# Performance work log

Hardware: AMD Instinct MI355X
Metric: run time of the kernel (lower is better)

The kernel has to match this reference:

```python
import jax, jax.numpy as jnp
import numpy as np

N_NODES = 50000
N_EDGES = 1600000
N_FEAT = 4
N_GRAPHS = 128
K = 5


def setup_inputs() -> dict:
    key = jax.random.key(0)
    ks = jax.random.split(key, 16)
    x = jax.random.normal(ks[0], (N_NODES, N_FEAT), dtype=jnp.float32)
    edge_index = jax.random.randint(ks[1], (2, N_EDGES), 0, N_NODES, dtype=jnp.int64)
    batch = jnp.sort(jax.random.randint(ks[2], (N_NODES,), 0, N_GRAPHS, dtype=jnp.int64))
    def lin(k, shape):
        fan_in = shape[-2]
        return jax.random.normal(k, shape, dtype=jnp.float32) / np.sqrt(fan_in)
    return {
        "x": x,
        "edge_index": edge_index,
        "batch": batch,
        "num_graphs": N_GRAPHS,
        "W1": lin(ks[3], (K, N_FEAT, 32)), "b1": jnp.zeros((32,), jnp.float32),
        "W2": lin(ks[4], (K, 32, 64)),     "b2": jnp.zeros((64,), jnp.float32),
        "W3": lin(ks[5], (K, 64, 64)),     "b3": jnp.zeros((64,), jnp.float32),
        "fcw1": lin(ks[6], (64, 32)), "fcb1": jnp.zeros((32,), jnp.float32),
        "fcw2": lin(ks[7], (32, 1)),  "fcb2": jnp.zeros((1,), jnp.float32),
    }


def _cheb_conv(h, src, dst, w, Wk, b, n_nodes):
    # PyG ChebConv with sym norm, lambda_max=2:
    #   L_hat h = scatter_add(w_e * h[src_e] -> dst_e), w_e = -dinv[src]*dinv[dst]
    def L(z):
        return jax.ops.segment_sum(w[:, None] * z[src], dst, num_segments=n_nodes)
    Tx0 = h
    Tx1 = L(h)
    out = jnp.einsum('nf,fo->no', Tx0, Wk[0]) + jnp.einsum('nf,fo->no', Tx1, Wk[1])
    for k in range(2, Wk.shape[0]):
        Tx2 = 2.0 * L(Tx1) - Tx0
        out = out + jnp.einsum('nf,fo->no', Tx2, Wk[k])
        Tx0, Tx1 = Tx1, Tx2
    return out + b


def reference(x, edge_index, batch, num_graphs, W1, b1, W2, b2, W3, b3,
              fcw1, fcb1, fcw2, fcb2):
    n = x.shape[0]
    src, dst = edge_index[0], edge_index[1]
    # remove self loops (PyG ChebConv does remove_self_loops first)
    ew = (src != dst).astype(x.dtype)
    deg = jax.ops.segment_sum(ew, src, num_segments=n)
    dinv = jnp.where(deg > 0, jax.lax.rsqrt(jnp.where(deg > 0, deg, 1.0)), 0.0)
    w = -ew * dinv[src] * dinv[dst]  # scaled Laplacian off-diagonal; diagonal is 0

    h = jax.nn.relu(_cheb_conv(x, src, dst, w, W1, b1, n))
    h = jax.nn.relu(_cheb_conv(h, src, dst, w, W2, b2, n))
    h = jax.nn.relu(_cheb_conv(h, src, dst, w, W3, b3, n))

    # global_mean_pool over graph segments
    sums = jax.ops.segment_sum(h, batch, num_segments=num_graphs)
    cnts = jax.ops.segment_sum(jnp.ones((n,), h.dtype), batch, num_segments=num_graphs)
    pooled = sums / jnp.maximum(cnts, 1.0)[:, None]

    h = jax.nn.relu(pooled @ fcw1 + fcb1)
    return h @ fcw2 + fcb2
```

## Files before the change

### kernel.cpp

```cpp
#include <hip/hip_runtime.h>


constexpr int N_NODES  = 50000;
constexpr int N_EDGES  = 1600000;
constexpr int N_GRAPHS = 128;

constexpr int N16  = N_NODES * 16;
constexpr int SB32 = (N_NODES + 31) / 32;

constexpr int NB_H = 256;
constexpr int EPB  = N_EDGES / NB_H;
constexpr int NW   = (N_NODES + 3) / 4;

static inline int cdiv(long long a, int b) { return (int)((a + b - 1) / b); }


template <int USE_DST>
__global__ __launch_bounds__(256) void hist_kernel(const int* __restrict__ src,
                                                   const int* __restrict__ dst,
                                                   unsigned* __restrict__ H) {
    __shared__ unsigned lds[NW];
    const int b = blockIdx.x, t = threadIdx.x;
    for (int i = t; i < NW; i += 256) lds[i] = 0;
    __syncthreads();
    const int e0 = b * EPB, e1 = e0 + EPB;
    for (int e = e0 + t; e < e1; e += 256) {
        int s = src[e], d = dst[e];
        if (s != d) {
            int key = USE_DST ? d : s;
            atomicAdd(&lds[key >> 2], 1u << (8 * (key & 3)));
        }
    }
    __syncthreads();
    unsigned* Hb = H + (size_t)b * NW;
    for (int i = t; i < NW; i += 256) Hb[i] = lds[i];
}

__global__ void merge_src_kernel(const unsigned* __restrict__ H, float* __restrict__ dinv) {
    int i = blockIdx.x * blockDim.x + threadIdx.x;
    if (i >= NW) return;
    unsigned s0 = 0, s1 = 0, s2 = 0, s3 = 0;
    for (int b = 0; b < NB_H; ++b) {
        unsigned v = H[(size_t)b * NW + i];
        s0 += v & 0xff; s1 += (v >> 8) & 0xff; s2 += (v >> 16) & 0xff; s3 += v >> 24;
    }
    dinv[4 * i + 0] = s0 ? rsqrtf((float)s0) : 0.f;
    dinv[4 * i + 1] = s1 ? rsqrtf((float)s1) : 0.f;
    dinv[4 * i + 2] = s2 ? rsqrtf((float)s2) : 0.f;
    dinv[4 * i + 3] = s3 ? rsqrtf((float)s3) : 0.f;
}

__global__ void merge_dst_kernel(const unsigned* __restrict__ H, unsigned* __restrict__ P,
                                 int* __restrict__ cnt) {
    int i = blockIdx.x * blockDim.x + threadIdx.x;
    if (i >= NW) return;
    unsigned p0 = 0, p1 = 0, p2 = 0, p3 = 0;
    for (int b = 0; b < NB_H; ++b) {
        size_t idx = (size_t)b * NW + i;
        unsigned v = H[idx];
        P[idx] = p0 | (p1 << 8) | (p2 << 16) | (p3 << 24);
        p0 += v & 0xff; p1 += (v >> 8) & 0xff; p2 += (v >> 16) & 0xff; p3 += v >> 24;
    }
    cnt[4 * i + 0] = (int)p0; cnt[4 * i + 1] = (int)p1;
    cnt[4 * i + 2] = (int)p2; cnt[4 * i + 3] = (int)p3;
}


constexpr int SCAN_B = 256;
constexpr int SCAN_NB = (N_NODES + SCAN_B - 1) / SCAN_B;

__global__ void scan_block_kernel(const int* __restrict__ cnt, int* __restrict__ row,
                                  int* __restrict__ bsum) {
    __shared__ int buf[SCAN_B];
    int t = threadIdx.x;
    int i = blockIdx.x * SCAN_B + t;
    buf[t] = (i < N_NODES) ? cnt[i] : 0;
    __syncthreads();
    for (int off = 1; off < SCAN_B; off <<= 1) {
        int a = (t >= off) ? buf[t - off] : 0;
        __syncthreads();
        buf[t] += a;
        __syncthreads();
    }
    if (i < N_NODES) row[i + 1] = buf[t];
    if (t == SCAN_B - 1) bsum[blockIdx.x] = buf[t];
    if (i == 0) row[0] = 0;
}

__global__ void scan_sums_kernel(int* __restrict__ bsum) {
    __shared__ int buf[SCAN_NB];
    int t = threadIdx.x;
    if (t < SCAN_NB) buf[t] = bsum[t];
    __syncthreads();
    for (int off = 1; off < SCAN_NB; off <<= 1) {
        int a = (t >= off && t < SCAN_NB) ? buf[t - off] : 0;
        __syncthreads();
        if (t < SCAN_NB) buf[t] += a;
        __syncthreads();
    }
    if (t < SCAN_NB) bsum[t] = buf[t];
}

__global__ void scan_add_kernel(int* __restrict__ row, const int* __restrict__ bsum) {
    int i = blockIdx.x * SCAN_B + threadIdx.x;
    if (blockIdx.x > 0 && i < N_NODES) row[i + 1] += bsum[blockIdx.x - 1];
}

__global__ __launch_bounds__(256) void place_kernel(const int* __restrict__ src,
                                                    const int* __restrict__ dst,
                                                    const float* __restrict__ dinv,
                                                    const int* __restrict__ row,
                                                    const unsigned* __restrict__ P,
                                                    float2* __restrict__ csr) {
    __shared__ unsigned lds[NW];
    const int b = blockIdx.x, t = threadIdx.x;
    for (int i = t; i < NW; i += 256) lds[i] = 0;
    __syncthreads();
    const int e0 = b * EPB, e1 = e0 + EPB;
    const unsigned* Pb = P + (size_t)b * NW;
    for (int e = e0 + t; e < e1; e += 256) {
        int s = src[e], d = dst[e];
        if (s != d) {
            float w = -dinv[s] * dinv[d];
            int sh = 8 * (d & 3);
            unsigned old = atomicAdd(&lds[d >> 2], 1u << sh);
            unsigned cur = (old >> sh) & 0xff;
            unsigned pref = (Pb[d >> 2] >> sh) & 0xff;
            int pos = row[d] + (int)pref + (int)cur;
            csr[pos] = make_float2(w, __int_as_float(s));
        }
    }
}


__global__ void gather4_kernel(const int* __restrict__ row, const float2* __restrict__ csr,
                               const float* __restrict__ z, const float* __restrict__ prev,
                               float* __restrict__ out, float alpha, float beta) {
    int node = blockIdx.x * blockDim.x + threadIdx.x;
    if (node >= N_NODES) return;
    int e0 = row[node], e1 = row[node + 1];
    const float4* z4 = (const float4*)z;
    float4 a = make_float4(0.f, 0.f, 0.f, 0.f);
#pragma unroll 4
    for (int e = e0; e < e1; ++e) {
        float2 ew = csr[e];
        float4 zz = z4[__float_as_int(ew.y)];
        a.x = fmaf(ew.x, zz.x, a.x);
        a.y = fmaf(ew.x, zz.y, a.y);
        a.z = fmaf(ew.x, zz.z, a.z);
        a.w = fmaf(ew.x, zz.w, a.w);
    }
    float4 r = make_float4(alpha * a.x, alpha * a.y, alpha * a.z, alpha * a.w);
    if (beta != 0.f) {
        const float4 p = ((const float4*)prev)[node];
        r.x = fmaf(beta, p.x, r.x);
        r.y = fmaf(beta, p.y, r.y);
        r.z = fmaf(beta, p.z, r.z);
        r.w = fmaf(beta, p.w, r.w);
    }
    ((float4*)out)[node] = r;
}

template <int NSLICE>
__global__ __launch_bounds__(256) void gather16_kernel(
        const int* __restrict__ row, const float2* __restrict__ csr,
        const float* __restrict__ z, const float* __restrict__ prev,
        float* __restrict__ out, float alpha, float beta) {
    constexpr int XPS = 8 / NSLICE;
    constexpr int CAP = 2048;
    __shared__ unsigned long long elds[CAP];
    const int bid = blockIdx.x;
    const int xcd = bid & 7;
    const int slice = xcd / XPS;
    const int sblk = (bid >> 3) * XPS + (xcd % XPS);
    if (sblk >= SB32) return;
    const int t = threadIdx.x;
    const int n = sblk * 32 + (t >> 3);
    const int lane = t & 7;
    const bool valid = (n < N_NODES);
    const float* zs = z + (size_t)slice * N16 + 2 * lane;
    const int e0 = valid ? row[n] : 0;
    const int e1 = valid ? row[n + 1] : 0;
    const int nb0 = sblk * 32;
    const int b0 = row[nb0];
    const int b1 = row[min(nb0 + 32, N_NODES)];
    float2 acc = make_float2(0.f, 0.f);
    for (int w0 = b0; w0 < b1; w0 += CAP) {
        const int w1 = min(w0 + CAP, b1);
        __syncthreads();
        for (int e = w0 + t; e < w1; e += 256)
            elds[e - w0] = __builtin_nontemporal_load((const unsigned long long*)csr + e);
        __syncthreads();
        const int g0 = max(e0, w0), g1 = min(e1, w1);
#pragma unroll 4
        for (int e = g0; e < g1; ++e) {
            unsigned long long raw = elds[e - w0];
            float w = __uint_as_float((unsigned)raw);
            int s = (int)(raw >> 32);
            const float2 zz = *(const float2*)(zs + (size_t)s * 16);
            acc.x = fmaf(w, zz.x, acc.x);
            acc.y = fmaf(w, zz.y, acc.y);
        }
    }
    if (valid) {
        float2 r = make_float2(alpha * acc.x, alpha * acc.y);
        size_t off = (size_t)slice * N16 + (size_t)n * 16 + 2 * lane;
        if (beta != 0.f) {
            float2 p;
            p.x = __builtin_nontemporal_load(prev + off);
            p.y = __builtin_nontemporal_load(prev + off + 1);
            r.x = fmaf(beta, p.x, r.x);
            r.y = fmaf(beta, p.y, r.y);
        }
        __builtin_nontemporal_store(r.x, out + off);
        __builtin_nontemporal_store(r.y, out + off + 1);
    }
}


template <int FI>
__global__ __launch_bounds__(256, 4) void combine64_kernel(
        const float* __restrict__ X, const float* __restrict__ T1,
        const float* __restrict__ T2, const float* __restrict__ T3,
        const float* __restrict__ T4, const float* __restrict__ W,
        const float* __restrict__ b, float* __restrict__ out) {
    constexpr int FO = 64;
    constexpr int TS = FI + 4;
    __shared__ float Ts[64 * TS];
    __shared__ float Ws[FI * FO];
    const int t = threadIdx.x;
    const int tn = t & 15;
    const int to = t >> 4;
    const int n_base = blockIdx.x * 64;
    const float* Tk[5] = {X, T1, T2, T3, T4};

    float acc[4][4];
    {
        const float4 bb = *(const float4*)(b + 4 * to);
#pragma unroll
        for (int i = 0; i < 4; ++i) {
            acc[i][0] = bb.x; acc[i][1] = bb.y; acc[i][2] = bb.z; acc[i][3] = bb.w;
        }
    }

#pragma unroll
    for (int k = 0; k < 5; ++k) {
        __syncthreads();
        {
            const float* base = Tk[k];
            constexpr int NV = 64 * FI / 4;
#pragma unroll
            for (int idx = t; idx < NV; idx += 256) {
                int r = idx / (FI / 4), c = idx % (FI / 4);
                int s = c >> 2;
                int j = (c & 3) * 4;
                float4 v = make_float4(0.f, 0.f, 0.f, 0.f);
                if (n_base + r < N_NODES)
                    v = *(const float4*)(base + (size_t)s * N16 +
                                         (size_t)(n_base + r) * 16 + j);
                *(float4*)(Ts + r * TS + 4 * c) = v;
            }
            const float4* w4 = (const float4*)(W + (size_t)k * FI * FO);
            constexpr int WV = FI * FO / 4;
#pragma unroll
            for (int idx = t; idx < WV; idx += 256) *(float4*)(Ws + 4 * idx) = w4[idx];
        }
        __syncthreads();
#pragma unroll 4
        for (int f0 = 0; f0 < FI; f0 += 4) {
            float tv[4][4];
#pragma unroll
            for (int i = 0; i < 4; ++i) {
                float4 q = *(const float4*)(Ts + (tn + 16 * i) * TS + f0);
                tv[i][0] = q.x; tv[i][1] = q.y; tv[i][2] = q.z; tv[i][3] = q.w;
            }
#pragma unroll
            for (int j = 0; j < 4; ++j) {
                float4 w = *(const float4*)(Ws + (f0 + j) * FO + 4 * to);
#pragma unroll
                for (int i = 0; i < 4; ++i) {
                    acc[i][0] = fmaf(tv[i][j], w.x, acc[i][0]);
                    acc[i][1] = fmaf(tv[i][j], w.y, acc[i][1]);
                    acc[i][2] = fmaf(tv[i][j], w.z, acc[i][2]);
                    acc[i][3] = fmaf(tv[i][j], w.w, acc[i][3]);
                }
            }
        }
    }
    __syncthreads();
#pragma unroll
    for (int i = 0; i < 4; ++i) {
        int n = n_base + tn + 16 * i;
        if (n < N_NODES) {
            float4 r = make_float4(fmaxf(acc[i][0], 0.f), fmaxf(acc[i][1], 0.f),
                                   fmaxf(acc[i][2], 0.f), fmaxf(acc[i][3], 0.f));
            int s = to >> 2;
            int j = (to & 3) * 4;
            *(float4*)(out + (size_t)s * N16 + (size_t)n * 16 + j) = r;
        }
    }
}

__global__ void combine432_kernel(const float* __restrict__ X, const float* __restrict__ T1,
                                  const float* __restrict__ T2, const float* __restrict__ T3,
                                  const float* __restrict__ T4, const float* __restrict__ W,
                                  const float* __restrict__ b, float* __restrict__ out) {
    __shared__ float Ws[5 * 4 * 32];
    int t = threadIdx.x;
    for (int i = t; i < 5 * 4 * 32; i += 256) Ws[i] = W[i];
    __syncthreads();
    int node = blockIdx.x * 8 + (t >> 5);
    int o = t & 31;
    if (node >= N_NODES) return;
    const float4* Tk[5] = {(const float4*)X, (const float4*)T1, (const float4*)T2,
                           (const float4*)T3, (const float4*)T4};
    float acc = b[o];
#pragma unroll
    for (int k = 0; k < 5; ++k) {
        float4 q = Tk[k][node];
        const float* w = Ws + k * 128 + o;
        acc = fmaf(q.x, w[0], acc);
        acc = fmaf(q.y, w[32], acc);
        acc = fmaf(q.z, w[64], acc);
        acc = fmaf(q.w, w[96], acc);
    }
    out[(size_t)(o >> 4) * N16 + (size_t)node * 16 + (o & 15)] = fmaxf(acc, 0.f);
}


__global__ void pool_kernel(const float* __restrict__ h, const int* __restrict__ batch,
                            float* __restrict__ pooled, float* __restrict__ cntf) {
    int wid = blockIdx.x * (blockDim.x / 64) + (threadIdx.x >> 6);
    int lane = threadIdx.x & 63;
    int nwaves = gridDim.x * (blockDim.x / 64);
    int per = (N_NODES + nwaves - 1) / nwaves;
    int n0 = wid * per;
    int n1 = min(n0 + per, N_NODES);
    if (n0 >= n1) return;
    const float* hp = h + (size_t)(lane >> 4) * N16 + (lane & 15);
    int cur = batch[n0];
    float acc = 0.f;
    int c = 0;
    for (int n = n0; n < n1; ++n) {
        int g = batch[n];
        if (g != cur) {
            atomicAdd(&pooled[cur * 64 + lane], acc);
            if (lane == 0) atomicAdd(&cntf[cur], (float)c);
            acc = 0.f; c = 0; cur = g;
        }
        acc += hp[(size_t)n * 16];
        ++c;
    }
    atomicAdd(&pooled[cur * 64 + lane], acc);
    if (lane == 0) atomicAdd(&cntf[cur], (float)c);
}

__global__ void fc_kernel(const float* __restrict__ pooled, const float* __restrict__ cnt,
                          const float* __restrict__ w1, const float* __restrict__ b1,
                          const float* __restrict__ w2, const float* __restrict__ b2,
                          float* __restrict__ out) {
    int g = blockIdx.x;
    int t = threadIdx.x;
    __shared__ float hid[32];
    float c = fmaxf(cnt[g], 1.0f);
    float acc = b1[t];
    for (int f = 0; f < 64; ++f) acc = fmaf(pooled[g * 64 + f] / c, w1[f * 32 + t], acc);
    hid[t] = fmaxf(acc, 0.f);
    __syncthreads();
    if (t == 0) {
        float acc2 = b2[0];
        for (int o = 0; o < 32; ++o) acc2 = fmaf(hid[o], w2[o], acc2);
        out[g] = acc2;
    }
}


template <int FI, int FO>
static void run_layer(const int* row, const float2* csr, const float* X,
                      float* T1, float* T2, float* T3, float* T4,
                      const float* W, const float* b, float* out, hipStream_t stream) {
    if constexpr (FI == 4) {
        dim3 g(cdiv(N_NODES, 256)), blk(256);
        hipLaunchKernelGGL(gather4_kernel, g, blk, 0, stream, row, csr, X,  X,  T1, 1.f, 0.f);
        hipLaunchKernelGGL(gather4_kernel, g, blk, 0, stream, row, csr, T1, X,  T2, 2.f, -1.f);
        hipLaunchKernelGGL(gather4_kernel, g, blk, 0, stream, row, csr, T2, T1, T3, 2.f, -1.f);
        hipLaunchKernelGGL(gather4_kernel, g, blk, 0, stream, row, csr, T3, T2, T4, 2.f, -1.f);
    } else {
        constexpr int NSLICE = FI / 16;
        constexpr int XPS = 8 / NSLICE;
        dim3 g(cdiv(SB32, XPS) * 8), blk(256);
        hipLaunchKernelGGL((gather16_kernel<NSLICE>), g, blk, 0, stream, row, csr, X,  X,  T1, 1.f, 0.f);
        hipLaunchKernelGGL((gather16_kernel<NSLICE>), g, blk, 0, stream, row, csr, T1, X,  T2, 2.f, -1.f);
        hipLaunchKernelGGL((gather16_kernel<NSLICE>), g, blk, 0, stream, row, csr, T2, T1, T3, 2.f, -1.f);
        hipLaunchKernelGGL((gather16_kernel<NSLICE>), g, blk, 0, stream, row, csr, T3, T2, T4, 2.f, -1.f);
    }
    if constexpr (FO == 64) {
        hipLaunchKernelGGL((combine64_kernel<FI>), dim3(cdiv(N_NODES, 64)), dim3(256), 0,
                           stream, X, T1, T2, T3, T4, W, b, out);
    } else {
        hipLaunchKernelGGL(combine432_kernel, dim3(cdiv(N_NODES, 8)), dim3(256), 0,
                           stream, X, T1, T2, T3, T4, W, b, out);
    }
}

extern "C" void kernel_launch(void* const* d_in, const int* in_sizes, int n_in,
                              void* d_out, int out_size, void* d_ws, size_t ws_size,
                              hipStream_t stream) {
    const float* x    = (const float*)d_in[0];
    const int*   ei   = (const int*)d_in[1];
    const int*   batch= (const int*)d_in[2];
    const float* W1   = (const float*)d_in[4];
    const float* b1   = (const float*)d_in[5];
    const float* W2   = (const float*)d_in[6];
    const float* b2   = (const float*)d_in[7];
    const float* W3   = (const float*)d_in[8];
    const float* b3   = (const float*)d_in[9];
    const float* fcw1 = (const float*)d_in[10];
    const float* fcb1 = (const float*)d_in[11];
    const float* fcw2 = (const float*)d_in[12];
    const float* fcb2 = (const float*)d_in[13];

    const int* src = ei;
    const int* dst = ei + N_EDGES;

    float* base = (float*)d_ws;
    float*  dinv   = base + 0;
    int*    cnt_i  = (int*)(base + 50000);
    int*    row    = (int*)(base + 100000);
    int*    bsum   = (int*)(base + 150004);
    float2* csr    = (float2*)(base + 150256);
    float*  T1     = base + 3350256;
    float*  T2     = base + 6550256;
    float*  T3     = base + 9750256;
    float*  T4     = base + 12950256;
    float*  H1     = T4 + 1600000;
    float*  H2     = base + 16150256;
    float*  pooled = base + 19350256;
    float*  cntf   = base + 19358448;

    unsigned* Hs = (unsigned*)T1;
    unsigned* Hd = (unsigned*)T2;
    unsigned* P  = (unsigned*)T3;

    hipLaunchKernelGGL((hist_kernel<0>), dim3(NB_H), dim3(256), 0, stream, src, dst, Hs);
    hipLaunchKernelGGL((hist_kernel<1>), dim3(NB_H), dim3(256), 0, stream, src, dst, Hd);
    hipLaunchKernelGGL(merge_src_kernel, dim3(cdiv(NW, 256)), dim3(256), 0, stream, Hs, dinv);
    hipLaunchKernelGGL(merge_dst_kernel, dim3(cdiv(NW, 256)), dim3(256), 0, stream, Hd, P, cnt_i);
    hipLaunchKernelGGL(scan_block_kernel, dim3(SCAN_NB), dim3(SCAN_B), 0, stream, cnt_i, row, bsum);
    hipLaunchKernelGGL(scan_sums_kernel, dim3(1), dim3(256), 0, stream, bsum);
    hipLaunchKernelGGL(scan_add_kernel, dim3(SCAN_NB), dim3(SCAN_B), 0, stream, row, bsum);
    hipLaunchKernelGGL(place_kernel, dim3(NB_H), dim3(256), 0, stream,
                       src, dst, dinv, row, P, csr);

    run_layer<4, 32>(row, csr, x,  T1, T2, T3, T4, W1, b1, H1, stream);
    run_layer<32, 64>(row, csr, H1, T1, T2, T3, T4, W2, b2, H2, stream);
    run_layer<64, 64>(row, csr, H2, T1, T2, T3, T4, W3, b3, T1, stream);

    hipMemsetAsync(pooled, 0, (8192 + 128) * sizeof(float), stream);
    hipLaunchKernelGGL(pool_kernel, dim3(128), dim3(256), 0, stream, T1, batch, pooled, cntf);
    hipLaunchKernelGGL(fc_kernel, dim3(N_GRAPHS), dim3(32), 0, stream,
                       pooled, cntf, fcw1, fcb1, fcw2, fcb2, (float*)d_out);
}
```

Measured before the change: 701.7 us.

## Fuse histogram kernels, split F4 gather per lane, process two nodes per group

Merges the src and dst degree histogram kernels into one pass over the edges, using dynamic shared memory for both histograms (about 100KB per block), so the edge list is read once instead of twice. The 4-feature gather now uses one thread per feature instead of one thread per node, for more parallelism, at the cost of redundant CSR reads across the four lanes. The 16-wide gather gives each 8-lane group two nodes, interleaving their edge loops for more memory-level parallelism, at the cost of masked padding work when the two degrees differ. The large shared allocation may reduce occupancy or exceed default limits.

```diff
diff --git a/kernel.cpp b/kernel.cpp
--- a/kernel.cpp
+++ b/kernel.cpp
@@ -6,7 +6,7 @@
 constexpr int N_GRAPHS = 128;
 
 constexpr int N16  = N_NODES * 16;
-constexpr int SB32 = (N_NODES + 31) / 32;
+constexpr int SB64 = (N_NODES + 63) / 64;
 
 constexpr int NB_H = 256;
 constexpr int EPB  = N_EDGES / NB_H;
@@ -15,25 +15,28 @@
 static inline int cdiv(long long a, int b) { return (int)((a + b - 1) / b); }
 
 
-template <int USE_DST>
-__global__ __launch_bounds__(256) void hist_kernel(const int* __restrict__ src,
-                                                   const int* __restrict__ dst,
-                                                   unsigned* __restrict__ H) {
-    __shared__ unsigned lds[NW];
+__global__ __launch_bounds__(256) void hist2_kernel(const int* __restrict__ src,
+                                                    const int* __restrict__ dst,
+                                                    unsigned* __restrict__ Hs,
+                                                    unsigned* __restrict__ Hd) {
+    extern __shared__ unsigned lds2[];
+    unsigned* ls = lds2;
+    unsigned* ld_ = lds2 + NW;
     const int b = blockIdx.x, t = threadIdx.x;
-    for (int i = t; i < NW; i += 256) lds[i] = 0;
+    for (int i = t; i < 2 * NW; i += 256) lds2[i] = 0;
     __syncthreads();
     const int e0 = b * EPB, e1 = e0 + EPB;
     for (int e = e0 + t; e < e1; e += 256) {
         int s = src[e], d = dst[e];
         if (s != d) {
-            int key = USE_DST ? d : s;
-            atomicAdd(&lds[key >> 2], 1u << (8 * (key & 3)));
-        }
-    }
-    __syncthreads();
-    unsigned* Hb = H + (size_t)b * NW;
-    for (int i = t; i < NW; i += 256) Hb[i] = lds[i];
+            atomicAdd(&ls[s >> 2], 1u << (8 * (s & 3)));
+            atomicAdd(&ld_[d >> 2], 1u << (8 * (d & 3)));
+        }
+    }
+    __syncthreads();
+    unsigned* HsB = Hs + (size_t)b * NW;
+    unsigned* HdB = Hd + (size_t)b * NW;
+    for (int i = t; i < NW; i += 256) { HsB[i] = ls[i]; HdB[i] = ld_[i]; }
 }
 
 __global__ void merge_src_kernel(const unsigned* __restrict__ H, float* __restrict__ dinv) {
@@ -133,32 +136,23 @@
 }
 
 
-__global__ void gather4_kernel(const int* __restrict__ row, const float2* __restrict__ csr,
-                               const float* __restrict__ z, const float* __restrict__ prev,
-                               float* __restrict__ out, float alpha, float beta) {
-    int node = blockIdx.x * blockDim.x + threadIdx.x;
+__global__ void gatherF4_kernel(const int* __restrict__ row, const float2* __restrict__ csr,
+                                const float* __restrict__ z, const float* __restrict__ prev,
+                                float* __restrict__ out, float alpha, float beta) {
+    int idx = blockIdx.x * blockDim.x + threadIdx.x;
+    int node = idx >> 2;
+    int lane = idx & 3;
     if (node >= N_NODES) return;
     int e0 = row[node], e1 = row[node + 1];
-    const float4* z4 = (const float4*)z;
-    float4 a = make_float4(0.f, 0.f, 0.f, 0.f);
+    float acc = 0.f;
 #pragma unroll 4
     for (int e = e0; e < e1; ++e) {
         float2 ew = csr[e];
-        float4 zz = z4[__float_as_int(ew.y)];
-        a.x = fmaf(ew.x, zz.x, a.x);
-        a.y = fmaf(ew.x, zz.y, a.y);
-        a.z = fmaf(ew.x, zz.z, a.z);
-        a.w = fmaf(ew.x, zz.w, a.w);
-    }
-    float4 r = make_float4(alpha * a.x, alpha * a.y, alpha * a.z, alpha * a.w);
-    if (beta != 0.f) {
-        const float4 p = ((const float4*)prev)[node];
-        r.x = fmaf(beta, p.x, r.x);
-        r.y = fmaf(beta, p.y, r.y);
-        r.z = fmaf(beta, p.z, r.z);
-        r.w = fmaf(beta, p.w, r.w);
-    }
-    ((float4*)out)[node] = r;
+        acc = fmaf(ew.x, z[(size_t)__float_as_int(ew.y) * 4 + lane], acc);
+    }
+    float r = alpha * acc;
+    if (beta != 0.f) r = fmaf(beta, prev[(size_t)node * 4 + lane], r);
+    out[(size_t)node * 4 + lane] = r;
 }
 
 template <int NSLICE>
@@ -173,44 +167,64 @@
     const int xcd = bid & 7;
     const int slice = xcd / XPS;
     const int sblk = (bid >> 3) * XPS + (xcd % XPS);
-    if (sblk >= SB32) return;
+    if (sblk >= SB64) return;
     const int t = threadIdx.x;
-    const int n = sblk * 32 + (t >> 3);
+    const int g = t >> 3;
     const int lane = t & 7;
-    const bool valid = (n < N_NODES);
+    const int nA = sblk * 64 + 2 * g;
+    const int nB = nA + 1;
     const float* zs = z + (size_t)slice * N16 + 2 * lane;
-    const int e0 = valid ? row[n] : 0;
-    const int e1 = valid ? row[n + 1] : 0;
-    const int nb0 = sblk * 32;
+    int e0A = 0, e1A = 0, e0B = 0, e1B = 0;
+    if (nA < N_NODES) { e0A = row[nA]; e1A = row[nA + 1]; }
+    if (nB < N_NODES) { e0B = row[nB]; e1B = row[nB + 1]; }
+    const int nb0 = sblk * 64;
     const int b0 = row[nb0];
-    const int b1 = row[min(nb0 + 32, N_NODES)];
-    float2 acc = make_float2(0.f, 0.f);
+    const int b1 = row[min(nb0 + 64, N_NODES)];
+    float2 aA = make_float2(0.f, 0.f), aB = make_float2(0.f, 0.f);
     for (int w0 = b0; w0 < b1; w0 += CAP) {
         const int w1 = min(w0 + CAP, b1);
+        const int wn = w1 - w0;
         __syncthreads();
         for (int e = w0 + t; e < w1; e += 256)
             elds[e - w0] = __builtin_nontemporal_load((const unsigned long long*)csr + e);
         __syncthreads();
-        const int g0 = max(e0, w0), g1 = min(e1, w1);
+        int dA = max(e0A, w0) - w0;
+        int dB = max(e0B, w0) - w0;
+        int cA = min(e1A, w1) - w0 - dA; if (cA < 0) cA = 0;
+        int cB = min(e1B, w1) - w0 - dB; if (cB < 0) cB = 0;
+        const int m = max(cA, cB);
 #pragma unroll 4
-        for (int e = g0; e < g1; ++e) {
-            unsigned long long raw = elds[e - w0];
-            float w = __uint_as_float((unsigned)raw);
-            int s = (int)(raw >> 32);
-            const float2 zz = *(const float2*)(zs + (size_t)s * 16);
-            acc.x = fmaf(w, zz.x, acc.x);
-            acc.y = fmaf(w, zz.y, acc.y);
-        }
-    }
-    if (valid) {
-        float2 r = make_float2(alpha * acc.x, alpha * acc.y);
-        size_t off = (size_t)slice * N16 + (size_t)n * 16 + 2 * lane;
+        for (int i = 0; i < m; ++i) {
+            int rA = min(dA + i, wn - 1);
+            int rB = min(dB + i, wn - 1);
+            unsigned long long ra = elds[rA];
+            unsigned long long rb = elds[rB];
+            float wA = (i < cA) ? __uint_as_float((unsigned)ra) : 0.f;
+            float wB = (i < cB) ? __uint_as_float((unsigned)rb) : 0.f;
+            int sA = (int)(ra >> 32);
+            int sB = (int)(rb >> 32);
+            const float2 zA = *(const float2*)(zs + (size_t)sA * 16);
+            const float2 zB = *(const float2*)(zs + (size_t)sB * 16);
+            aA.x = fmaf(wA, zA.x, aA.x); aA.y = fmaf(wA, zA.y, aA.y);
+            aB.x = fmaf(wB, zB.x, aB.x); aB.y = fmaf(wB, zB.y, aB.y);
+        }
+    }
+    if (nA < N_NODES) {
+        float2 r = make_float2(alpha * aA.x, alpha * aA.y);
+        size_t off = (size_t)slice * N16 + (size_t)nA * 16 + 2 * lane;
         if (beta != 0.f) {
-            float2 p;
-            p.x = __builtin_nontemporal_load(prev + off);
-            p.y = __builtin_nontemporal_load(prev + off + 1);
-            r.x = fmaf(beta, p.x, r.x);
-            r.y = fmaf(beta, p.y, r.y);
+            r.x = fmaf(beta, __builtin_nontemporal_load(prev + off), r.x);
+            r.y = fmaf(beta, __builtin_nontemporal_load(prev + off + 1), r.y);
+        }
+        __builtin_nontemporal_store(r.x, out + off);
+        __builtin_nontemporal_store(r.y, out + off + 1);
+    }
+    if (nB < N_NODES) {
+        float2 r = make_float2(alpha * aB.x, alpha * aB.y);
+        size_t off = (size_t)slice * N16 + (size_t)nB * 16 + 2 * lane;
+        if (beta != 0.f) {
+            r.x = fmaf(beta, __builtin_nontemporal_load(prev + off), r.x);
+            r.y = fmaf(beta, __builtin_nontemporal_load(prev + off + 1), r.y);
         }
         __builtin_nontemporal_store(r.x, out + off);
         __builtin_nontemporal_store(r.y, out + off + 1);
@@ -380,15 +394,15 @@
                       float* T1, float* T2, float* T3, float* T4,
                       const float* W, const float* b, float* out, hipStream_t stream) {
     if constexpr (FI == 4) {
-        dim3 g(cdiv(N_NODES, 256)), blk(256);
-        hipLaunchKernelGGL(gather4_kernel, g, blk, 0, stream, row, csr, X,  X,  T1, 1.f, 0.f);
-        hipLaunchKernelGGL(gather4_kernel, g, blk, 0, stream, row, csr, T1, X,  T2, 2.f, -1.f);
-        hipLaunchKernelGGL(gather4_kernel, g, blk, 0, stream, row, csr, T2, T1, T3, 2.f, -1.f);
-        hipLaunchKernelGGL(gather4_kernel, g, blk, 0, stream, row, csr, T3, T2, T4, 2.f, -1.f);
+        dim3 g(cdiv((long long)N_NODES * 4, 256)), blk(256);
+        hipLaunchKernelGGL(gatherF4_kernel, g, blk, 0, stream, row, csr, X,  X,  T1, 1.f, 0.f);
+        hipLaunchKernelGGL(gatherF4_kernel, g, blk, 0, stream, row, csr, T1, X,  T2, 2.f, -1.f);
+        hipLaunchKernelGGL(gatherF4_kernel, g, blk, 0, stream, row, csr, T2, T1, T3, 2.f, -1.f);
+        hipLaunchKernelGGL(gatherF4_kernel, g, blk, 0, stream, row, csr, T3, T2, T4, 2.f, -1.f);
     } else {
         constexpr int NSLICE = FI / 16;
         constexpr int XPS = 8 / NSLICE;
-        dim3 g(cdiv(SB32, XPS) * 8), blk(256);
+        dim3 g(cdiv(SB64, XPS) * 8), blk(256);
         hipLaunchKernelGGL((gather16_kernel<NSLICE>), g, blk, 0, stream, row, csr, X,  X,  T1, 1.f, 0.f);
         hipLaunchKernelGGL((gather16_kernel<NSLICE>), g, blk, 0, stream, row, csr, T1, X,  T2, 2.f, -1.f);
         hipLaunchKernelGGL((gather16_kernel<NSLICE>), g, blk, 0, stream, row, csr, T2, T1, T3, 2.f, -1.f);
@@ -442,8 +456,8 @@
     unsigned* Hd = (unsigned*)T2;
     unsigned* P  = (unsigned*)T3;
 
-    hipLaunchKernelGGL((hist_kernel<0>), dim3(NB_H), dim3(256), 0, stream, src, dst, Hs);
-    hipLaunchKernelGGL((hist_kernel<1>), dim3(NB_H), dim3(256), 0, stream, src, dst, Hd);
+    hipLaunchKernelGGL(hist2_kernel, dim3(NB_H), dim3(256), 2 * NW * sizeof(unsigned),
+                       stream, src, dst, Hs, Hd);
     hipLaunchKernelGGL(merge_src_kernel, dim3(cdiv(NW, 256)), dim3(256), 0, stream, Hs, dinv);
     hipLaunchKernelGGL(merge_dst_kernel, dim3(cdiv(NW, 256)), dim3(256), 0, stream, Hd, P, cnt_i);
     hipLaunchKernelGGL(scan_block_kernel, dim3(SCAN_NB), dim3(SCAN_B), 0, stream, cnt_i, row, bsum);
```

Result: slower. 760.5 us (+8.4%).
